# Kernel tuning notes

Hardware: AMD Instinct MI355X
Metric: run time of the kernel (lower is better)

Reference implementation:

```python
import jax, jax.numpy as jnp
import numpy as np

LN_EPS = 1e-12


def layer_norm(x, g, b):
    mu = jnp.mean(x, axis=-1, keepdims=True)
    var = jnp.mean(jnp.square(x - mu), axis=-1, keepdims=True)
    return (x - mu) * jax.lax.rsqrt(var + LN_EPS) * g + b


def setup_inputs() -> dict:
    key = jax.random.key(0)
    ks = jax.random.split(key, 12)
    B, L, H, P, V = 8, 512, 768, 200, 30522
    src_scores = jax.random.normal(ks[0], (B, L, L), jnp.float32)
    seq_hidden = jax.random.normal(ks[1], (B, L, H), jnp.float32)
    seq_mask = jax.random.randint(ks[2], (B, L), 0, 2).astype(jnp.float32)
    pos_emb = jax.random.normal(ks[3], (512, P), jnp.float32) * 0.02
    Wp = jax.random.normal(ks[4], (H, P), jnp.float32) * 0.02
    bp = jnp.zeros((H,), jnp.float32)
    Wt = jax.random.normal(ks[5], (H, H), jnp.float32) * 0.02
    bt = jnp.zeros((H,), jnp.float32)
    ln_g = jnp.ones((H,), jnp.float32)
    ln_b = jnp.zeros((H,), jnp.float32)
    Wd = jax.random.normal(ks[6], (V, H), jnp.float32) * 0.02
    dec_bias = jnp.zeros((V,), jnp.float32)
    return dict(src_scores=src_scores, seq_hidden=seq_hidden, seq_mask=seq_mask,
                pos_emb=pos_emb, Wp=Wp, bp=bp, Wt=Wt, bt=bt,
                ln_g=ln_g, ln_b=ln_b, Wd=Wd, dec_bias=dec_bias)


def reference(src_scores, seq_hidden, seq_mask, pos_emb, Wp, bp, Wt, bt, ln_g, ln_b, Wd, dec_bias):
    L = src_scores.shape[1]
    # position embeddings for first L positions, projected to hidden size: [L, H]
    pos_h = pos_emb[:L] @ Wp.T + bp
    # pos_scores[b, l, s] = pos_h[l] . seq_hidden[b, s]
    pos_scores = jnp.einsum('lh,bsh->bls', pos_h, seq_hidden)
    scores = pos_scores + src_scores + seq_mask[:, None, :] * -10000.0
    alpha = jax.nn.softmax(scores, axis=-1)                 # [B, L, L]
    seq_sum = jnp.einsum('bls,bsh->blh', alpha, seq_hidden)  # [B, L, H]
    # BertPredictionHeadTransform: dense -> gelu (exact) -> LayerNorm
    h = layer_norm(jax.nn.gelu(seq_sum @ Wt.T + bt, approximate=False), ln_g, ln_b)
    target_scores = h @ Wd.T + dec_bias                      # [B, L, V]
    return target_scores
```

## Files before the change

kernel.cpp:

```cpp
#include <hip/hip_runtime.h>

using f32x4  = __attribute__((ext_vector_type(4))) float;
using short8 = __attribute__((ext_vector_type(8))) short;
using short4v= __attribute__((ext_vector_type(4))) short;
typedef __attribute__((ext_vector_type(8))) __bf16 bf16x8;

__device__ static inline short f2bf(float f){
    unsigned u = __builtin_bit_cast(unsigned, f);
    u += 0x7fffu + ((u >> 16) & 1u);
    return (short)(u >> 16);
}

__device__ static inline void gload_lds16(const void* g, void* l){
    __builtin_amdgcn_global_load_lds(
        (const __attribute__((address_space(1))) void*)g,
        (__attribute__((address_space(3))) void*)l, 16, 0, 0);
}

#define BKK 64

template<int EPI, bool T2D>
__global__ __launch_bounds__(256, 2)
void gemm_bt(const short* __restrict__ A, const short* __restrict__ B,
             float* __restrict__ outF, short* __restrict__ outB,
             const float* __restrict__ bias,
             const float* __restrict__ addmat, const float* __restrict__ mask,
             int K, int ldc, int Ncheck,
             long sA, long sB, long sC, long sX, int maskStride)
{
    __shared__ short Abuf[128*BKK];
    __shared__ short Bbuf[128*BKK];
    const int tid  = threadIdx.x;
    const int wave = tid >> 6;
    const int lane = tid & 63;
    const int bz   = blockIdx.z;

    int bx = blockIdx.x, by = blockIdx.y;
    if constexpr (T2D) {
        const int GX = gridDim.x, GY = gridDim.y;
        const int f  = blockIdx.y * GX + blockIdx.x;
        const int nfull  = GX >> 3;
        const int fullsz = (nfull << 3) * GY;
        int mg, mloc, nloc, nbase;
        if (f < fullsz) {
            const int band = f / (GY << 3);
            const int r    = f - band * (GY << 3);
            mg   = r >> 6;
            const int rr = r & 63;
            mloc = rr & 7; nloc = rr >> 3;
            nbase = band << 3;
        } else {
            const int rem = GX & 7;
            const int fp  = f - fullsz;
            const int gsz = rem << 3;
            mg   = fp / gsz;
            const int rr = fp - mg * gsz;
            mloc = rr & 7; nloc = rr >> 3;
            nbase = nfull << 3;
        }
        bx = nbase + nloc;
        by = (mg << 3) + mloc;
    }
    const int m0 = by * 128;
    const int n0 = bx * 128;
    const short* Ab = A + (long)bz * sA;
    const short* Bb = B + (long)bz * sB;

    const int wr = (wave >> 1) * 64;
    const int wc = (wave &  1) * 64;

    f32x4 acc[4][4];
    #pragma unroll
    for (int i=0;i<4;++i)
        #pragma unroll
        for (int j=0;j<4;++j) acc[i][j] = (f32x4){0.f,0.f,0.f,0.f};

    const int srow = wave*32 + (lane >> 3);
    const int kch  = (lane & 7) ^ (lane >> 3);
    const short* gA = Ab + (long)(m0 + srow)*K + kch*8;
    const short* gB = Bb + (long)(n0 + srow)*K + kch*8;
    short* lA = Abuf + wave*32*BKK;
    short* lB = Bbuf + wave*32*BKK;

    for (int k0 = 0; k0 < K; k0 += BKK) {
        __syncthreads();
        #pragma unroll
        for (int is=0; is<4; ++is){
            gload_lds16(gA + k0 + (long)is*8*K, lA + is*8*BKK);
            gload_lds16(gB + k0 + (long)is*8*K, lB + is*8*BKK);
        }
        __syncthreads();
        #pragma unroll
        for (int ks=0; ks<2; ++ks){
            bf16x8 af[4], bfr[4];
            const int chunk = ks*4 + (lane >> 4);
            #pragma unroll
            for (int mi=0;mi<4;++mi){
                int row = wr + mi*16 + (lane & 15);
                af[mi] = *(const bf16x8*)((const char*)Abuf + row*128 + ((chunk ^ (row & 7))<<4));
            }
            #pragma unroll
            for (int ni=0;ni<4;++ni){
                int row = wc + ni*16 + (lane & 15);
                bfr[ni] = *(const bf16x8*)((const char*)Bbuf + row*128 + ((chunk ^ (row & 7))<<4));
            }
            #pragma unroll
            for (int mi=0;mi<4;++mi)
                #pragma unroll
                for (int ni=0;ni<4;++ni)
                    acc[mi][ni] = __builtin_amdgcn_mfma_f32_16x16x32_bf16(af[mi], bfr[ni], acc[mi][ni], 0, 0, 0);
        }
    }

    const int rb = (lane >> 4) * 4;
    const int cb = lane & 15;
    #pragma unroll
    for (int mi=0;mi<4;++mi){
        #pragma unroll
        for (int r=0;r<4;++r){
            const int row = m0 + wr + mi*16 + rb + r;
            #pragma unroll
            for (int ni=0;ni<4;++ni){
                const int col = n0 + wc + ni*16 + cb;
                float v = acc[mi][ni][r];
                if constexpr (EPI == 0) {
                    v += addmat[(long)bz*sX + (long)row*ldc + col]
                         - 10000.f * mask[bz*maskStride + col];
                    outF[(long)bz*sC + (long)row*ldc + col] = v;
                } else if constexpr (EPI == 1) {
                    outB[(long)bz*sC + (long)row*ldc + col] = f2bf(v);
                } else if constexpr (EPI == 3) {
                    if (col < Ncheck) outF[(long)row*ldc + col] = v + bias[col];
                } else if constexpr (EPI == 4) {
                    outB[(long)row*ldc + col] = f2bf(v + bias[col]);
                }
            }
        }
    }
}

__global__ __launch_bounds__(256)
void conv_bf16(const float* __restrict__ in, short* __restrict__ out, long n, long ntot)
{
    const long stride = (long)gridDim.x * 2048;
    for (long i = ((long)blockIdx.x*256 + threadIdx.x)*8; i < ntot; i += stride){
        short8 o = (short8){0,0,0,0,0,0,0,0};
        if (i < n){
            f32x4 a = *(const f32x4*)(in + i);
            f32x4 b = *(const f32x4*)(in + i + 4);
            o[0]=f2bf(a[0]); o[1]=f2bf(a[1]); o[2]=f2bf(a[2]); o[3]=f2bf(a[3]);
            o[4]=f2bf(b[0]); o[5]=f2bf(b[1]); o[6]=f2bf(b[2]); o[7]=f2bf(b[3]);
        }
        *(short8*)(out + i) = o;
    }
}

__global__ __launch_bounds__(256)
void conv_pad(const float* __restrict__ in, short* __restrict__ out,
              int Cin, int Cpad, int total)
{
    int idx = blockIdx.x*256 + threadIdx.x;
    if (idx >= total) return;
    int r = idx / Cpad, c = idx - r*Cpad;
    short v = 0;
    if (c < Cin) v = f2bf(in[(long)r*Cin + c]);
    out[idx] = v;
}

__global__ __launch_bounds__(256)
void transpose_to_bf16(const float* __restrict__ in, short* __restrict__ out, int R, int C)
{
    __shared__ float t[32][33];
    const long boff = (long)blockIdx.z * R * C;
    const float* inb = in + boff;
    short* outb = out + boff;
    int c0 = blockIdx.x*32, r0 = blockIdx.y*32;
    int tx = threadIdx.x & 31, ty = threadIdx.x >> 5;
    #pragma unroll
    for (int j=0;j<32;j+=8) t[ty+j][tx] = inb[(long)(r0+ty+j)*C + c0+tx];
    __syncthreads();
    #pragma unroll
    for (int j=0;j<32;j+=8) outb[(long)(c0+ty+j)*R + r0+tx] = f2bf(t[tx][ty+j]);
}

__global__ __launch_bounds__(256)
void softmax_bf16(const float* __restrict__ scores, short* __restrict__ alpha, int L)
{
    const int row  = blockIdx.x*4 + (threadIdx.x >> 6);
    const int lane = threadIdx.x & 63;
    const float* p = scores + (long)row*L + lane*8;
    f32x4 v0 = *(const f32x4*)p;
    f32x4 v1 = *(const f32x4*)(p+4);
    float x[8] = {v0[0],v0[1],v0[2],v0[3],v1[0],v1[1],v1[2],v1[3]};
    float m = x[0];
    #pragma unroll
    for (int j=1;j<8;++j) m = fmaxf(m, x[j]);
    #pragma unroll
    for (int off=32; off; off>>=1) m = fmaxf(m, __shfl_xor(m, off));
    float s = 0.f;
    #pragma unroll
    for (int j=0;j<8;++j){ x[j] = __expf(x[j]-m); s += x[j]; }
    #pragma unroll
    for (int off=32; off; off>>=1) s += __shfl_xor(s, off);
    const float rinv = 1.f / s;
    short8 o;
    #pragma unroll
    for (int j=0;j<8;++j) o[j] = f2bf(x[j]*rinv);
    *(short8*)(alpha + (long)row*L + lane*8) = o;
}

__global__ __launch_bounds__(256)
void gelu_ln(const float* __restrict__ lin, short* __restrict__ h,
             const float* __restrict__ g, const float* __restrict__ b, int H)
{
    const int row  = blockIdx.x*4 + (threadIdx.x >> 6);
    const int lane = threadIdx.x & 63;
    const float* p = lin + (long)row*H;
    float x[12];
    #pragma unroll
    for (int c=0;c<3;++c){
        f32x4 v = *(const f32x4*)(p + c*256 + lane*4);
        x[c*4+0]=v[0]; x[c*4+1]=v[1]; x[c*4+2]=v[2]; x[c*4+3]=v[3];
    }
    float sum=0.f, sq=0.f;
    #pragma unroll
    for (int j=0;j<12;++j){
        float t = 0.5f * x[j] * (1.f + erff(x[j]*0.70710678118654752f));
        x[j] = t; sum += t; sq += t*t;
    }
    #pragma unroll
    for (int off=32; off; off>>=1){ sum += __shfl_xor(sum, off); sq += __shfl_xor(sq, off); }
    const float mu  = sum * (1.f/768.f);
    const float var = sq  * (1.f/768.f) - mu*mu;
    const float inv = rsqrtf(var + 1e-12f);
    #pragma unroll
    for (int c=0;c<3;++c){
        short4v o;
        #pragma unroll
        for (int j=0;j<4;++j){
            int col = c*256 + lane*4 + j;
            o[j] = f2bf((x[c*4+j]-mu)*inv*g[col] + b[col]);
        }
        *(short4v*)(h + (long)row*H + c*256 + lane*4) = o;
    }
}

extern "C" void kernel_launch(void* const* d_in, const int* in_sizes, int n_in,
                              void* d_out, int out_size, void* d_ws, size_t ws_size,
                              hipStream_t stream)
{
    const float* src_scores = (const float*)d_in[0];
    const float* seq_hidden = (const float*)d_in[1];
    const float* seq_mask   = (const float*)d_in[2];
    const float* pos_emb    = (const float*)d_in[3];
    const float* Wp         = (const float*)d_in[4];
    const float* bp         = (const float*)d_in[5];
    const float* Wt         = (const float*)d_in[6];
    const float* bt         = (const float*)d_in[7];
    const float* ln_g       = (const float*)d_in[8];
    const float* ln_b       = (const float*)d_in[9];
    const float* Wd         = (const float*)d_in[10];
    const float* dec_bias   = (const float*)d_in[11];
    float* out = (float*)d_out;

    const int B=8, L=512, H=768, V=30522, Vp=30592, Kp=256;

    const size_t need = ((size_t)Vp*H + (size_t)B*L*H) * sizeof(short);
    if (ws_size < need) return;
    short* wd_bf = (short*)d_ws;
    short* h_bf  = wd_bf + (long)Vp*H;

    char* sc = (char*)d_out;
    short* sh_nat = (short*)sc;  sc += (long)B*L*H*2;
    short* sh_t   = (short*)sc;  sc += (long)B*L*H*2;
    short* pe_p   = (short*)sc;  sc += (long)L*Kp*2;
    short* wp_p   = (short*)sc;  sc += (long)H*Kp*2;
    short* pos_h  = (short*)sc;  sc += (long)L*H*2;
    short* wt_bf  = (short*)sc;  sc += (long)H*H*2;
    float* scoresb= (float*)sc;  sc += (long)B*L*L*4;
    short* alpha  = (short*)sc;  sc += (long)B*L*L*2;
    short* seqsum = (short*)sc;  sc += (long)B*L*H*2;
    float* lin5   = (float*)sc;  sc += (long)B*L*H*4;

    {   long n=(long)V*H, ntot=(long)Vp*H;
        int blocks=(int)((ntot+2047)/2048); if (blocks>2048) blocks=2048;
        conv_bf16<<<dim3(blocks),256,0,stream>>>(Wd, wd_bf, n, ntot); }
    {   long n=(long)H*H; int blocks=(int)((n+2047)/2048);
        conv_bf16<<<dim3(blocks),256,0,stream>>>(Wt, wt_bf, n, n); }
    {   long n=(long)B*L*H; int blocks=(int)((n+2047)/2048); if (blocks>2048) blocks=2048;
        conv_bf16<<<dim3(blocks),256,0,stream>>>(seq_hidden, sh_nat, n, n); }
    transpose_to_bf16<<<dim3(H/32, L/32, B),256,0,stream>>>(seq_hidden, sh_t, L, H);
    {   int total=L*Kp;
        conv_pad<<<dim3((total+255)/256),256,0,stream>>>(pos_emb, pe_p, 200, Kp, total); }
    {   int total=H*Kp;
        conv_pad<<<dim3((total+255)/256),256,0,stream>>>(Wp, wp_p, 200, Kp, total); }

    gemm_bt<4,false><<<dim3(H/128, L/128, 1),256,0,stream>>>(
        pe_p, wp_p, nullptr, pos_h, bp, nullptr, nullptr,
        Kp, H, H, 0L, 0L, 0L, 0L, 0);

    gemm_bt<0,false><<<dim3(L/128, L/128, B),256,0,stream>>>(
        pos_h, sh_nat, scoresb, nullptr, nullptr, src_scores, seq_mask,
        H, L, L, 0L, (long)L*H, (long)L*L, (long)L*L, L);

    softmax_bf16<<<dim3(B*L/4),256,0,stream>>>(scoresb, alpha, L);

    gemm_bt<1,false><<<dim3(H/128, L/128, B),256,0,stream>>>(
        alpha, sh_t, nullptr, seqsum, nullptr, nullptr, nullptr,
        L, H, H, (long)L*L, (long)H*L, (long)L*H, 0L, 0);

    gemm_bt<3,false><<<dim3(H/128, (B*L)/128, 1),256,0,stream>>>(
        seqsum, wt_bf, lin5, nullptr, bt, nullptr, nullptr,
        H, H, H, 0L, 0L, 0L, 0L, 0);

    gelu_ln<<<dim3(B*L/4),256,0,stream>>>(lin5, h_bf, ln_g, ln_b, H);

    gemm_bt<3,true><<<dim3(Vp/128, (B*L)/128, 1),256,0,stream>>>(
        h_bf, wd_bf, out, nullptr, dec_bias, nullptr, nullptr,
        H, V, V, 0L, 0L, 0L, 0L, 0);
}
```

Baseline: 473.2 us.

## Use 256x256 tile GEMM with 512 threads for vocab decoder projection

Adds a new bf16 MFMA GEMM kernel with 256x256 output tiles, 8 waves of 128x64 each, a K-step of 32 with double-buffered direct-to-LDS loads, and swizzled LDS reads. The kernel replaces the 128x128 tiled GEMM for the large decoder projection (4096x30522x768). It also clamps B rows at the padded edge and remaps blocks in a grouped order for L2 reuse. The larger tile raises arithmetic intensity per LDS byte, at the cost of higher register pressure (128 accumulator floats per lane) and possible occupancy or tail-wave imbalance.

```diff
diff --git a/kernel.cpp b/kernel.cpp
--- a/kernel.cpp
+++ b/kernel.cpp
@@ -139,6 +139,110 @@
     }
 }
 
+template<bool T2D>
+__global__ __launch_bounds__(512, 2)
+void gemm_bt256(const short* __restrict__ A, const short* __restrict__ B,
+                float* __restrict__ outF, const float* __restrict__ bias,
+                int K, int ldc, int Ncheck, int maxBrow)
+{
+    __shared__ __align__(16) short Abuf[2][256*32];
+    __shared__ __align__(16) short Bbuf[2][256*32];
+    const int tid  = threadIdx.x;
+    const int wave = tid >> 6;
+    const int lane = tid & 63;
+
+    int bx = blockIdx.x, by = blockIdx.y;
+    if constexpr (T2D) {
+        const int GX = gridDim.x, GY = gridDim.y;
+        const int f  = blockIdx.y * GX + blockIdx.x;
+        const int band = f / (GY << 3);
+        const int r2   = f - band * (GY << 3);
+        const int mg   = r2 >> 6;
+        const int rr   = r2 & 63;
+        bx = (band << 3) + (rr >> 3);
+        by = (mg << 3) + (rr & 7);
+    }
+    const int m0 = by * 256;
+    const int n0 = bx * 256;
+
+    const int wr = (wave >> 2) * 128;
+    const int wc = (wave & 3) * 64;
+
+    f32x4 acc[8][4];
+    #pragma unroll
+    for (int i=0;i<8;++i)
+        #pragma unroll
+        for (int j=0;j<4;++j) acc[i][j] = (f32x4){0.f,0.f,0.f,0.f};
+
+    const int srow = wave*16 + (lane >> 2);
+    const int kch  = (lane & 3) ^ ((lane >> 3) & 3);
+    const short* gA0 = A + (long)(m0 + srow)       * K + kch*8;
+    const short* gA1 = A + (long)(m0 + 128 + srow) * K + kch*8;
+    int br0 = n0 + srow;        if (br0 > maxBrow) br0 = maxBrow;
+    int br1 = n0 + 128 + srow;  if (br1 > maxBrow) br1 = maxBrow;
+    const short* gB0 = B + (long)br0 * K + kch*8;
+    const short* gB1 = B + (long)br1 * K + kch*8;
+    const int lofs = wave*16*32;
+
+    const int nt = K / 32;
+
+    auto STAGE = [&](int buf, int t){
+        const long k0 = (long)t * 32;
+        gload_lds16(gA0 + k0, &Abuf[buf][lofs]);
+        gload_lds16(gA1 + k0, &Abuf[buf][128*32 + lofs]);
+        gload_lds16(gB0 + k0, &Bbuf[buf][lofs]);
+        gload_lds16(gB1 + k0, &Bbuf[buf][128*32 + lofs]);
+    };
+
+    STAGE(0, 0);
+
+    const int qsl = (((lane >> 4) ^ ((lane >> 1) & 3)) << 4);
+    const int rA  = wr + (lane & 15);
+    const int rB  = wc + (lane & 15);
+
+    for (int t = 0; t < nt; ++t) {
+        const int cur = t & 1, nxt = cur ^ 1;
+        __builtin_amdgcn_s_barrier();
+        if (t + 1 < nt) {
+            STAGE(nxt, t + 1);
+            asm volatile("s_waitcnt vmcnt(4)" ::: "memory");
+        } else {
+            asm volatile("s_waitcnt vmcnt(0)" ::: "memory");
+        }
+        __builtin_amdgcn_s_barrier();
+        asm volatile("" ::: "memory");
+
+        bf16x8 af[8], bfr[4];
+        #pragma unroll
+        for (int ni=0;ni<4;++ni)
+            bfr[ni] = *(const bf16x8*)((const char*)&Bbuf[cur][0] + (rB + ni*16)*64 + qsl);
+        #pragma unroll
+        for (int mi=0;mi<8;++mi)
+            af[mi]  = *(const bf16x8*)((const char*)&Abuf[cur][0] + (rA + mi*16)*64 + qsl);
+        #pragma unroll
+        for (int mi=0;mi<8;++mi)
+            #pragma unroll
+            for (int ni=0;ni<4;++ni)
+                acc[mi][ni] = __builtin_amdgcn_mfma_f32_16x16x32_bf16(af[mi], bfr[ni], acc[mi][ni], 0, 0, 0);
+    }
+
+    const int rb = (lane >> 4) * 4;
+    const int cb = lane & 15;
+    #pragma unroll
+    for (int mi=0;mi<8;++mi){
+        #pragma unroll
+        for (int r=0;r<4;++r){
+            const long row = (long)m0 + wr + mi*16 + rb + r;
+            #pragma unroll
+            for (int ni=0;ni<4;++ni){
+                const int col = n0 + wc + ni*16 + cb;
+                if (col < Ncheck)
+                    outF[row*ldc + col] = acc[mi][ni][r] + bias[col];
+            }
+        }
+    }
+}
+
 __global__ __launch_bounds__(256)
 void conv_bf16(const float* __restrict__ in, short* __restrict__ out, long n, long ntot)
 {
@@ -315,7 +419,6 @@
 
     gelu_ln<<<dim3(B*L/4),256,0,stream>>>(lin5, h_bf, ln_g, ln_b, H);
 
-    gemm_bt<3,true><<<dim3(Vp/128, (B*L)/128, 1),256,0,stream>>>(
-        h_bf, wd_bf, out, nullptr, dec_bias, nullptr, nullptr,
-        H, V, V, 0L, 0L, 0L, 0L, 0);
-}
+    gemm_bt256<true><<<dim3(120, 16), 512, 0, stream>>>(
+        h_bf, wd_bf, out, dec_bias, H, V, V, Vp - 1);
+}
```

New measurement: 557.5 us. 1.18x slower.
